# Kernel tuning notes

Measured on AMD Instinct MI355X. Metric: run time of the kernel, lower is better.

## Reference

```python
import jax, jax.numpy as jnp
import numpy as np

EMB = 1024
HEAD = 64

def setup_inputs() -> dict:
    key = jax.random.key(0)
    ks = jax.random.split(key, 7)
    s = 1.0 / np.sqrt(EMB)
    x = jax.random.normal(ks[0], (4, 2048, EMB), dtype=jnp.float32)
    Wq = jax.random.uniform(ks[1], (EMB, HEAD), jnp.float32, -s, s)
    bq = jax.random.uniform(ks[2], (HEAD,), jnp.float32, -s, s)
    Wk = jax.random.uniform(ks[3], (EMB, HEAD), jnp.float32, -s, s)
    bk = jax.random.uniform(ks[4], (HEAD,), jnp.float32, -s, s)
    Wv = jax.random.uniform(ks[5], (EMB, HEAD), jnp.float32, -s, s)
    bv = jax.random.uniform(ks[6], (HEAD,), jnp.float32, -s, s)
    return {"x": x, "Wq": Wq, "bq": bq, "Wk": Wk, "bk": bk, "Wv": Wv, "bv": bv}

def reference(x, Wq, bq, Wk, bk, Wv, bv):
    x = x.astype(jnp.float32)
    q = jnp.einsum('bse,ed->bsd', x, Wq) + bq  # [B,S,H]
    k = jnp.einsum('bse,ed->bsd', x, Wk) + bk
    v = jnp.einsum('bse,ed->bsd', x, Wv) + bv
    scale = 1.0 / jnp.sqrt(jnp.asarray(k.shape[-1], jnp.float32))
    scores = jnp.einsum('bqd,bkd->bqk', q, k) * scale  # [B,S,S]
    attn = jax.nn.softmax(scores, axis=-1)
    return jnp.einsum('bqk,bkd->bqd', attn, v)  # [B,S,H]
```

## Files before the change

kernel.cpp:

```cpp
#include <hip/hip_runtime.h>
#include <hip/hip_bf16.h>

#define ROWS_TOTAL 8192
#define EMB 1024
#define HEAD 64
#define SEQ 2048
#define KSPLIT 8
#define KC (SEQ / KSPLIT)
#define KT 64

typedef __attribute__((ext_vector_type(8))) short short8;
typedef __attribute__((ext_vector_type(4))) float f32x4;

#define MFMA16(a, b, c) __builtin_amdgcn_mfma_f32_16x16x32_bf16((a), (b), (c), 0, 0, 0)

static __device__ __forceinline__ unsigned short f2bf(float f) {
    union { float f; unsigned u; } v; v.f = f;
    unsigned r = v.u + 0x7fff + ((v.u >> 16) & 1);
    return (unsigned short)(r >> 16);
}

static __device__ __forceinline__ unsigned pk2(float a, float b) {
    __hip_bfloat162 h = __float22bfloat162_rn(float2{a, b});
    union { __hip_bfloat162 h; unsigned u; } v; v.h = h;
    return v.u;
}

__global__ __launch_bounds__(256) void wprep_kernel(
    const float* __restrict__ Wq, const float* __restrict__ Wk,
    const float* __restrict__ Wv, unsigned short* __restrict__ Wf)
{
    __shared__ float Tr[64][65];
    const int m  = blockIdx.y;
    const int k0 = blockIdx.x * 64;
    const float* __restrict__ W = (m == 0) ? Wq : (m == 1) ? Wk : Wv;
    const int t = threadIdx.x;

    #pragma unroll
    for (int j = 0; j < 4; ++j) {
        int flat = j * 1024 + t * 4;
        int k = flat >> 6, n = flat & 63;
        float4 w4 = *(const float4*)&W[(size_t)(k0 + k) * 64 + n];
        Tr[n + 0][k] = w4.x; Tr[n + 1][k] = w4.y;
        Tr[n + 2][k] = w4.z; Tr[n + 3][k] = w4.w;
    }
    __syncthreads();

    const int n   = t >> 2;
    const int k16 = t & 3;
    union { short8 s; unsigned u[4]; } o0, o1;
    #pragma unroll
    for (int i = 0; i < 4; ++i) {
        o0.u[i] = pk2(Tr[n][k16 * 16 + 2 * i],     Tr[n][k16 * 16 + 2 * i + 1]);
        o1.u[i] = pk2(Tr[n][k16 * 16 + 8 + 2 * i], Tr[n][k16 * 16 + 9 + 2 * i]);
    }
    const int tile = m * 4 + (n >> 4);
    const int ln   = n & 15;
    const int kc32 = (k0 >> 5) + (k16 >> 1);
    const int half = k16 & 1;
    size_t off = ((size_t)(kc32 * 12 + tile) * 16 + ln) * 32 + half * 16;
    *(short8*)&Wf[off]     = o0.s;
    *(short8*)&Wf[off + 8] = o1.s;
}

__global__ __launch_bounds__(512) void qkv_mfma(
    const float* __restrict__ x, const unsigned short* __restrict__ Wf,
    const float* __restrict__ bq, const float* __restrict__ bk,
    const float* __restrict__ bv,
    unsigned short* __restrict__ Qb, unsigned short* __restrict__ Kb,
    unsigned short* __restrict__ Vt)
{
    __shared__ unsigned short Xl[16][136];
    __shared__ f32x4 pr[4][3][64];
    __shared__ unsigned short vlds[64][20];

    const int t    = threadIdx.x;
    const int w    = t >> 6;
    const int lane = t & 63;
    const int ln   = lane & 15;
    const int quad = lane >> 4;
    const int m0   = blockIdx.x * 16;
    const int cg   = w >> 1;
    const int kh   = w & 1;

    const f32x4 zero = (f32x4){0.f, 0.f, 0.f, 0.f};
    f32x4 acc[3];
    #pragma unroll
    for (int j = 0; j < 3; ++j) acc[j] = zero;

    const int srow = t >> 5;
    const int scol = (t & 31) * 4;
    const float* __restrict__ xsrc = x + (size_t)(m0 + srow) * EMB + scol;

    for (int kt = 0; kt < EMB; kt += 128) {
        float4 xv = *(const float4*)(xsrc + kt);
        uint2 pk; pk.x = pk2(xv.x, xv.y); pk.y = pk2(xv.z, xv.w);
        *(uint2*)&Xl[srow][scol] = pk;
        __syncthreads();

        #pragma unroll
        for (int cc = 0; cc < 2; ++cc) {
            short8 af = *(const short8*)&Xl[ln][kh * 64 + cc * 32 + quad * 8];
            const int kc32 = (kt >> 5) + kh * 2 + cc;
            #pragma unroll
            for (int j = 0; j < 3; ++j) {
                const int tile = cg * 3 + j;
                const unsigned short* wp =
                    Wf + ((size_t)(kc32 * 12 + tile) * 16 + ln) * 32 + quad * 8;
                short8 bf = *(const short8*)wp;
                acc[j] = MFMA16(af, bf, acc[j]);
            }
        }
        __syncthreads();
    }

    if (kh == 1) {
        #pragma unroll
        for (int j = 0; j < 3; ++j) pr[cg][j][lane] = acc[j];
    }
    __syncthreads();

    if (kh == 0) {
        const float qs = 0.125f * 1.44269504f;
        #pragma unroll
        for (int j = 0; j < 3; ++j) {
            acc[j] += pr[cg][j][lane];
            const int tile = cg * 3 + j;
            const int mat  = tile >> 2;
            const int d    = (tile & 3) * 16 + ln;
            const float* bp = (mat == 0) ? bq : (mat == 1) ? bk : bv;
            const float bias = bp[d];
            #pragma unroll
            for (int r = 0; r < 4; ++r) {
                float vfull = acc[j][r] + bias;
                int row = m0 + quad * 4 + r;
                if (mat == 0)      Qb[(size_t)row * 64 + d] = f2bf(vfull * qs);
                else if (mat == 1) Kb[(size_t)row * 64 + d] = f2bf(vfull);
                else               vlds[d][quad * 4 + r] = f2bf(vfull);
            }
        }
    }
    __syncthreads();

    if (t < 256) {
        const int b  = m0 >> 11;
        const int s0 = m0 & 2047;
        const int d  = t >> 2;
        const int sq = (t & 3) * 4;
        ushort4 pk = {vlds[d][sq + 0], vlds[d][sq + 1],
                      vlds[d][sq + 2], vlds[d][sq + 3]};
        *(ushort4*)&Vt[((size_t)b * 64 + d) * SEQ + s0 + sq] = pk;
    }
}

__global__ __launch_bounds__(512) void attn_mfma(
    const unsigned short* __restrict__ Qb, const unsigned short* __restrict__ Kb,
    const unsigned short* __restrict__ Vt,
    float* __restrict__ Opart, float* __restrict__ lpart)
{
    __shared__ unsigned short Kl[KT][72];
    __shared__ unsigned short Vl[HEAD][72];
    __shared__ unsigned short Plds[8][16][72];

    const int t    = threadIdx.x;
    const int w    = t >> 6;
    const int lane = t & 63;
    const int ln   = lane & 15;
    const int quad = lane >> 4;

    const int c  = blockIdx.y;
    const int q0 = blockIdx.x * 128 + w * 16;
    const int b  = blockIdx.x >> 4;

    const unsigned short* qbase = Qb + (size_t)(q0 + ln) * 64 + quad * 8;
    short8 qa0 = *(const short8*)(qbase);
    short8 qa1 = *(const short8*)(qbase + 32);

    const f32x4 zero = (f32x4){0.f, 0.f, 0.f, 0.f};
    f32x4 O[4];
    #pragma unroll
    for (int j = 0; j < 4; ++j) O[j] = zero;
    float lacc[4] = {0.f, 0.f, 0.f, 0.f};

    const int skey = t >> 3;
    const int soff = (t & 7) * 8;
    const unsigned short* Ksrc =
        Kb + ((size_t)b * SEQ + c * KC + skey) * 64 + soff;
    const unsigned short* Vsrc =
        Vt + ((size_t)b * 64 + skey) * SEQ + c * KC + soff;

    unsigned short* P = &Plds[w][0][0];

    for (int kt = 0; kt < KC; kt += KT) {
        *(short8*)&Kl[skey][soff] = *(const short8*)(Ksrc + (size_t)kt * 64);
        *(short8*)&Vl[skey][soff] = *(const short8*)(Vsrc + kt);
        __syncthreads();

        f32x4 s[4];
        #pragma unroll
        for (int sub = 0; sub < 4; ++sub) {
            short8 kb0 = *(const short8*)&Kl[sub * 16 + ln][quad * 8];
            short8 kb1 = *(const short8*)&Kl[sub * 16 + ln][32 + quad * 8];
            s[sub] = MFMA16(qa0, kb0, zero);
            s[sub] = MFMA16(qa1, kb1, s[sub]);
        }

        #pragma unroll
        for (int r = 0; r < 4; ++r) {
            float p0 = __builtin_amdgcn_exp2f(s[0][r]);
            float p1 = __builtin_amdgcn_exp2f(s[1][r]);
            float p2 = __builtin_amdgcn_exp2f(s[2][r]);
            float p3 = __builtin_amdgcn_exp2f(s[3][r]);
            lacc[r] += (p0 + p1) + (p2 + p3);
            unsigned u01 = pk2(p0, p1);
            unsigned u23 = pk2(p2, p3);
            unsigned short* prow = P + (quad * 4 + r) * 72;
            prow[ln]      = (unsigned short)u01;
            prow[16 + ln] = (unsigned short)(u01 >> 16);
            prow[32 + ln] = (unsigned short)u23;
            prow[48 + ln] = (unsigned short)(u23 >> 16);
        }
        short8 pa0 = *(const short8*)&Plds[w][ln][quad * 8];
        short8 pa1 = *(const short8*)&Plds[w][ln][32 + quad * 8];

        #pragma unroll
        for (int j = 0; j < 4; ++j) {
            short8 vb0 = *(const short8*)&Vl[j * 16 + ln][quad * 8];
            short8 vb1 = *(const short8*)&Vl[j * 16 + ln][32 + quad * 8];
            O[j] = MFMA16(pa0, vb0, O[j]);
            O[j] = MFMA16(pa1, vb1, O[j]);
        }
        __syncthreads();
    }

    #pragma unroll
    for (int m = 1; m < 16; m <<= 1) {
        #pragma unroll
        for (int r = 0; r < 4; ++r) lacc[r] += __shfl_xor(lacc[r], m);
    }

    float* __restrict__ ob = Opart + ((size_t)c * ROWS_TOTAL + q0) * 64;
    #pragma unroll
    for (int j = 0; j < 4; ++j)
        #pragma unroll
        for (int r = 0; r < 4; ++r)
            ob[(size_t)(quad * 4 + r) * 64 + j * 16 + ln] = O[j][r];

    if (ln == 0) {
        #pragma unroll
        for (int r = 0; r < 4; ++r)
            lpart[(size_t)c * ROWS_TOTAL + q0 + quad * 4 + r] = lacc[r];
    }
}

__global__ __launch_bounds__(256) void reduce_kernel(
    const float* __restrict__ Opart, const float* __restrict__ lpart,
    float* __restrict__ out)
{
    const int idx = blockIdx.x * 256 + threadIdx.x;
    const int r   = idx >> 6;
    float osum = 0.f, lsum = 0.f;
    #pragma unroll
    for (int c = 0; c < KSPLIT; ++c) {
        osum += Opart[(size_t)c * ROWS_TOTAL * HEAD + idx];
        lsum += lpart[(size_t)c * ROWS_TOTAL + r];
    }
    out[idx] = osum / lsum;
}

extern "C" void kernel_launch(void* const* d_in, const int* in_sizes, int n_in,
                              void* d_out, int out_size, void* d_ws, size_t ws_size,
                              hipStream_t stream)
{
    const float* x  = (const float*)d_in[0];
    const float* Wq = (const float*)d_in[1];
    const float* bq = (const float*)d_in[2];
    const float* Wk = (const float*)d_in[3];
    const float* bk = (const float*)d_in[4];
    const float* Wv = (const float*)d_in[5];
    const float* bv = (const float*)d_in[6];
    float* out = (float*)d_out;

    char* ws = (char*)d_ws;
    unsigned short* Qb = (unsigned short*)ws;
    unsigned short* Kb = Qb + (size_t)ROWS_TOTAL * HEAD;
    unsigned short* Vt = Kb + (size_t)ROWS_TOTAL * HEAD;
    unsigned short* Wf = Vt + (size_t)ROWS_TOTAL * HEAD;
    float* lpart = (float*)(Wf + (size_t)3 * HEAD * EMB);
    float* Opart = lpart + (size_t)KSPLIT * ROWS_TOTAL;

    wprep_kernel<<<dim3(16, 3), 256, 0, stream>>>(Wq, Wk, Wv, Wf);
    qkv_mfma<<<dim3(512), 512, 0, stream>>>(x, Wf, bq, bk, bv, Qb, Kb, Vt);
    attn_mfma<<<dim3(64, KSPLIT), 512, 0, stream>>>(Qb, Kb, Vt, Opart, lpart);
    reduce_kernel<<<dim3((ROWS_TOTAL * HEAD) / 256), 256, 0, stream>>>(Opart, lpart, out);
}
```

Before: 118.8 us.

## Double rows per QKV block and prefetch global loads into registers

```diff
diff --git a/kernel.cpp b/kernel.cpp
--- a/kernel.cpp
+++ b/kernel.cpp
@@ -70,45 +70,57 @@
     unsigned short* __restrict__ Qb, unsigned short* __restrict__ Kb,
     unsigned short* __restrict__ Vt)
 {
-    __shared__ unsigned short Xl[16][136];
-    __shared__ f32x4 pr[4][3][64];
-    __shared__ unsigned short vlds[64][20];
+    __shared__ union {
+        unsigned short Xl[32][136];
+        f32x4 pr[4][3][2][64];
+    } sh;
+    __shared__ unsigned short vlds[64][36];
 
     const int t    = threadIdx.x;
     const int w    = t >> 6;
     const int lane = t & 63;
     const int ln   = lane & 15;
     const int quad = lane >> 4;
-    const int m0   = blockIdx.x * 16;
+    const int m0   = blockIdx.x * 32;
     const int cg   = w >> 1;
     const int kh   = w & 1;
 
     const f32x4 zero = (f32x4){0.f, 0.f, 0.f, 0.f};
-    f32x4 acc[3];
-    #pragma unroll
-    for (int j = 0; j < 3; ++j) acc[j] = zero;
-
-    const int srow = t >> 5;
-    const int scol = (t & 31) * 4;
+    f32x4 acc[3][2];
+    #pragma unroll
+    for (int j = 0; j < 3; ++j) { acc[j][0] = zero; acc[j][1] = zero; }
+
+    const int srow = t >> 4;
+    const int scol = (t & 15) * 8;
     const float* __restrict__ xsrc = x + (size_t)(m0 + srow) * EMB + scol;
 
+    float4 xa = *(const float4*)(xsrc);
+    float4 xb = *(const float4*)(xsrc + 4);
+
     for (int kt = 0; kt < EMB; kt += 128) {
-        float4 xv = *(const float4*)(xsrc + kt);
-        uint2 pk; pk.x = pk2(xv.x, xv.y); pk.y = pk2(xv.z, xv.w);
-        *(uint2*)&Xl[srow][scol] = pk;
+        union { short8 s; unsigned u[4]; } xp;
+        xp.u[0] = pk2(xa.x, xa.y); xp.u[1] = pk2(xa.z, xa.w);
+        xp.u[2] = pk2(xb.x, xb.y); xp.u[3] = pk2(xb.z, xb.w);
+        *(short8*)&sh.Xl[srow][scol] = xp.s;
         __syncthreads();
 
+        if (kt + 128 < EMB) {
+            xa = *(const float4*)(xsrc + kt + 128);
+            xb = *(const float4*)(xsrc + kt + 132);
+        }
+
         #pragma unroll
         for (int cc = 0; cc < 2; ++cc) {
-            short8 af = *(const short8*)&Xl[ln][kh * 64 + cc * 32 + quad * 8];
+            short8 af0 = *(const short8*)&sh.Xl[ln][kh * 64 + cc * 32 + quad * 8];
+            short8 af1 = *(const short8*)&sh.Xl[16 + ln][kh * 64 + cc * 32 + quad * 8];
             const int kc32 = (kt >> 5) + kh * 2 + cc;
             #pragma unroll
             for (int j = 0; j < 3; ++j) {
                 const int tile = cg * 3 + j;
-                const unsigned short* wp =
-                    Wf + ((size_t)(kc32 * 12 + tile) * 16 + ln) * 32 + quad * 8;
-                short8 bf = *(const short8*)wp;
-                acc[j] = MFMA16(af, bf, acc[j]);
+                short8 bf = *(const short8*)
+                    (Wf + ((size_t)(kc32 * 12 + tile) * 16 + ln) * 32 + quad * 8);
+                acc[j][0] = MFMA16(af0, bf, acc[j][0]);
+                acc[j][1] = MFMA16(af1, bf, acc[j][1]);
             }
         }
         __syncthreads();
@@ -116,7 +128,10 @@
 
     if (kh == 1) {
         #pragma unroll
-        for (int j = 0; j < 3; ++j) pr[cg][j][lane] = acc[j];
+        for (int j = 0; j < 3; ++j) {
+            sh.pr[cg][j][0][lane] = acc[j][0];
+            sh.pr[cg][j][1][lane] = acc[j][1];
+        }
     }
     __syncthreads();
 
@@ -124,29 +139,33 @@
         const float qs = 0.125f * 1.44269504f;
         #pragma unroll
         for (int j = 0; j < 3; ++j) {
-            acc[j] += pr[cg][j][lane];
             const int tile = cg * 3 + j;
             const int mat  = tile >> 2;
             const int d    = (tile & 3) * 16 + ln;
             const float* bp = (mat == 0) ? bq : (mat == 1) ? bk : bv;
             const float bias = bp[d];
             #pragma unroll
-            for (int r = 0; r < 4; ++r) {
-                float vfull = acc[j][r] + bias;
-                int row = m0 + quad * 4 + r;
-                if (mat == 0)      Qb[(size_t)row * 64 + d] = f2bf(vfull * qs);
-                else if (mat == 1) Kb[(size_t)row * 64 + d] = f2bf(vfull);
-                else               vlds[d][quad * 4 + r] = f2bf(vfull);
+            for (int rg = 0; rg < 2; ++rg) {
+                f32x4 s = acc[j][rg];
+                s += sh.pr[cg][j][rg][lane];
+                #pragma unroll
+                for (int r = 0; r < 4; ++r) {
+                    float vfull = s[r] + bias;
+                    int row = m0 + rg * 16 + quad * 4 + r;
+                    if (mat == 0)      Qb[(size_t)row * 64 + d] = f2bf(vfull * qs);
+                    else if (mat == 1) Kb[(size_t)row * 64 + d] = f2bf(vfull);
+                    else               vlds[d][rg * 16 + quad * 4 + r] = f2bf(vfull);
+                }
             }
         }
     }
     __syncthreads();
 
-    if (t < 256) {
+    {
         const int b  = m0 >> 11;
         const int s0 = m0 & 2047;
-        const int d  = t >> 2;
-        const int sq = (t & 3) * 4;
+        const int d  = t >> 3;
+        const int sq = (t & 7) * 4;
         ushort4 pk = {vlds[d][sq + 0], vlds[d][sq + 1],
                       vlds[d][sq + 2], vlds[d][sq + 3]};
         *(ushort4*)&Vt[((size_t)b * 64 + d) * SEQ + s0 + sq] = pk;
@@ -191,10 +210,18 @@
 
     unsigned short* P = &Plds[w][0][0];
 
+    short8 kreg = *(const short8*)(Ksrc);
+    short8 vreg = *(const short8*)(Vsrc);
+
     for (int kt = 0; kt < KC; kt += KT) {
-        *(short8*)&Kl[skey][soff] = *(const short8*)(Ksrc + (size_t)kt * 64);
-        *(short8*)&Vl[skey][soff] = *(const short8*)(Vsrc + kt);
+        *(short8*)&Kl[skey][soff] = kreg;
+        *(short8*)&Vl[skey][soff] = vreg;
         __syncthreads();
+
+        if (kt + KT < KC) {
+            kreg = *(const short8*)(Ksrc + (size_t)(kt + KT) * 64);
+            vreg = *(const short8*)(Vsrc + kt + KT);
+        }
 
         f32x4 s[4];
         #pragma unroll
@@ -290,7 +317,7 @@
     float* Opart = lpart + (size_t)KSPLIT * ROWS_TOTAL;
 
     wprep_kernel<<<dim3(16, 3), 256, 0, stream>>>(Wq, Wk, Wv, Wf);
-    qkv_mfma<<<dim3(512), 512, 0, stream>>>(x, Wf, bq, bk, bv, Qb, Kb, Vt);
+    qkv_mfma<<<dim3(256), 512, 0, stream>>>(x, Wf, bq, bk, bv, Qb, Kb, Vt);
     attn_mfma<<<dim3(64, KSPLIT), 512, 0, stream>>>(Qb, Kb, Vt, Opart, lpart);
     reduce_kernel<<<dim3((ROWS_TOTAL * HEAD) / 256), 256, 0, stream>>>(Opart, lpart, out);
 }
```

New measurement: 121.8 us. 2.5% more time.

## Store K and V in MFMA fragment layout and read them directly from global

Applied to the files above, without the earlier changes.

```diff
diff --git a/kernel.cpp b/kernel.cpp
--- a/kernel.cpp
+++ b/kernel.cpp
@@ -7,7 +7,6 @@
 #define SEQ 2048
 #define KSPLIT 8
 #define KC (SEQ / KSPLIT)
-#define KT 64
 
 typedef __attribute__((ext_vector_type(8))) short short8;
 typedef __attribute__((ext_vector_type(4))) float f32x4;
@@ -25,6 +24,7 @@
     union { __hip_bfloat162 h; unsigned u; } v; v.h = h;
     return v.u;
 }
+
 
 __global__ __launch_bounds__(256) void wprep_kernel(
     const float* __restrict__ Wq, const float* __restrict__ Wk,
@@ -67,8 +67,8 @@
     const float* __restrict__ x, const unsigned short* __restrict__ Wf,
     const float* __restrict__ bq, const float* __restrict__ bk,
     const float* __restrict__ bv,
-    unsigned short* __restrict__ Qb, unsigned short* __restrict__ Kb,
-    unsigned short* __restrict__ Vt)
+    unsigned short* __restrict__ Qb, unsigned short* __restrict__ Kf,
+    unsigned short* __restrict__ Vf)
 {
     __shared__ unsigned short Xl[16][136];
     __shared__ f32x4 pr[4][3][64];
@@ -105,9 +105,8 @@
             #pragma unroll
             for (int j = 0; j < 3; ++j) {
                 const int tile = cg * 3 + j;
-                const unsigned short* wp =
-                    Wf + ((size_t)(kc32 * 12 + tile) * 16 + ln) * 32 + quad * 8;
-                short8 bf = *(const short8*)wp;
+                short8 bf = *(const short8*)
+                    (Wf + ((size_t)(kc32 * 12 + tile) * 16 + ln) * 32 + quad * 8);
                 acc[j] = MFMA16(af, bf, acc[j]);
             }
         }
@@ -120,8 +119,12 @@
     }
     __syncthreads();
 
+    const int b2 = m0 >> 11;
+    const int s0 = m0 & 2047;
+
     if (kh == 0) {
         const float qs = 0.125f * 1.44269504f;
+        const int st = s0 >> 4;
         #pragma unroll
         for (int j = 0; j < 3; ++j) {
             acc[j] += pr[cg][j][lane];
@@ -134,33 +137,38 @@
             for (int r = 0; r < 4; ++r) {
                 float vfull = acc[j][r] + bias;
                 int row = m0 + quad * 4 + r;
-                if (mat == 0)      Qb[(size_t)row * 64 + d] = f2bf(vfull * qs);
-                else if (mat == 1) Kb[(size_t)row * 64 + d] = f2bf(vfull);
-                else               vlds[d][quad * 4 + r] = f2bf(vfull);
+                if (mat == 0) {
+                    Qb[(size_t)row * 64 + d] = f2bf(vfull * qs);
+                } else if (mat == 1) {
+                    size_t off = ((((size_t)(b2 * 128 + st) * 2 + (d >> 5)) * 16
+                                   + (quad * 4 + r)) * 4 + ((d >> 3) & 3)) * 8 + (d & 7);
+                    Kf[off] = f2bf(vfull);
+                } else {
+                    vlds[d][quad * 4 + r] = f2bf(vfull);
+                }
             }
         }
     }
     __syncthreads();
 
     if (t < 256) {
-        const int b  = m0 >> 11;
-        const int s0 = m0 & 2047;
         const int d  = t >> 2;
-        const int sq = (t & 3) * 4;
-        ushort4 pk = {vlds[d][sq + 0], vlds[d][sq + 1],
-                      vlds[d][sq + 2], vlds[d][sq + 3]};
-        *(ushort4*)&Vt[((size_t)b * 64 + d) * SEQ + s0 + sq] = pk;
+        const int kq = (t & 3) * 4;
+        const int key = s0 + kq;
+        ushort4 pk = {vlds[d][kq + 0], vlds[d][kq + 1],
+                      vlds[d][kq + 2], vlds[d][kq + 3]};
+        size_t off = ((((size_t)(b2 * 64 + (key >> 5)) * 4 + (d >> 4)) * 16
+                       + (d & 15)) * 4 + ((key >> 3) & 3)) * 8 + (key & 7);
+        *(ushort4*)&Vf[off] = pk;
     }
 }
 
 __global__ __launch_bounds__(512) void attn_mfma(
-    const unsigned short* __restrict__ Qb, const unsigned short* __restrict__ Kb,
-    const unsigned short* __restrict__ Vt,
+    const unsigned short* __restrict__ Qb, const unsigned short* __restrict__ Kf,
+    const unsigned short* __restrict__ Vf,
     float* __restrict__ Opart, float* __restrict__ lpart)
 {
-    __shared__ unsigned short Kl[KT][72];
-    __shared__ unsigned short Vl[HEAD][72];
-    __shared__ unsigned short Plds[8][16][72];
+    __shared__ unsigned short Plds[8][16][40];
 
     const int t    = threadIdx.x;
     const int w    = t >> 6;
@@ -182,55 +190,42 @@
     for (int j = 0; j < 4; ++j) O[j] = zero;
     float lacc[4] = {0.f, 0.f, 0.f, 0.f};
 
-    const int skey = t >> 3;
-    const int soff = (t & 7) * 8;
-    const unsigned short* Ksrc =
-        Kb + ((size_t)b * SEQ + c * KC + skey) * 64 + soff;
-    const unsigned short* Vsrc =
-        Vt + ((size_t)b * 64 + skey) * SEQ + c * KC + soff;
-
+    const int lnq = (ln * 4 + quad) * 8;
+    const unsigned short* Kfb = Kf + (size_t)b * 128 * 1024;
+    const unsigned short* Vfb = Vf + (size_t)b * 64 * 2048;
     unsigned short* P = &Plds[w][0][0];
 
-    for (int kt = 0; kt < KC; kt += KT) {
-        *(short8*)&Kl[skey][soff] = *(const short8*)(Ksrc + (size_t)kt * 64);
-        *(short8*)&Vl[skey][soff] = *(const short8*)(Vsrc + kt);
-        __syncthreads();
-
-        f32x4 s[4];
-        #pragma unroll
-        for (int sub = 0; sub < 4; ++sub) {
-            short8 kb0 = *(const short8*)&Kl[sub * 16 + ln][quad * 8];
-            short8 kb1 = *(const short8*)&Kl[sub * 16 + ln][32 + quad * 8];
-            s[sub] = MFMA16(qa0, kb0, zero);
-            s[sub] = MFMA16(qa1, kb1, s[sub]);
-        }
+    for (int kt = 0; kt < KC; kt += 32) {
+        const int gk    = c * KC + kt;
+        const int ktile = gk >> 4;
+        const int kch   = gk >> 5;
+
+        short8 k00 = *(const short8*)(Kfb + (size_t)ktile * 1024 + lnq);
+        short8 k01 = *(const short8*)(Kfb + (size_t)ktile * 1024 + 512 + lnq);
+        short8 k10 = *(const short8*)(Kfb + (size_t)(ktile + 1) * 1024 + lnq);
+        short8 k11 = *(const short8*)(Kfb + (size_t)(ktile + 1) * 1024 + 512 + lnq);
+
+        f32x4 sA = MFMA16(qa0, k00, zero); sA = MFMA16(qa1, k01, sA);
+        f32x4 sB = MFMA16(qa0, k10, zero); sB = MFMA16(qa1, k11, sB);
 
         #pragma unroll
         for (int r = 0; r < 4; ++r) {
-            float p0 = __builtin_amdgcn_exp2f(s[0][r]);
-            float p1 = __builtin_amdgcn_exp2f(s[1][r]);
-            float p2 = __builtin_amdgcn_exp2f(s[2][r]);
-            float p3 = __builtin_amdgcn_exp2f(s[3][r]);
-            lacc[r] += (p0 + p1) + (p2 + p3);
-            unsigned u01 = pk2(p0, p1);
-            unsigned u23 = pk2(p2, p3);
-            unsigned short* prow = P + (quad * 4 + r) * 72;
-            prow[ln]      = (unsigned short)u01;
-            prow[16 + ln] = (unsigned short)(u01 >> 16);
-            prow[32 + ln] = (unsigned short)u23;
-            prow[48 + ln] = (unsigned short)(u23 >> 16);
-        }
-        short8 pa0 = *(const short8*)&Plds[w][ln][quad * 8];
-        short8 pa1 = *(const short8*)&Plds[w][ln][32 + quad * 8];
+            float pA = __builtin_amdgcn_exp2f(sA[r]);
+            float pB = __builtin_amdgcn_exp2f(sB[r]);
+            lacc[r] += pA + pB;
+            unsigned u = pk2(pA, pB);
+            unsigned short* prow = P + (quad * 4 + r) * 40;
+            prow[ln]      = (unsigned short)u;
+            prow[16 + ln] = (unsigned short)(u >> 16);
+        }
+        short8 pa = *(const short8*)&Plds[w][ln][quad * 8];
 
         #pragma unroll
         for (int j = 0; j < 4; ++j) {
-            short8 vb0 = *(const short8*)&Vl[j * 16 + ln][quad * 8];
-            short8 vb1 = *(const short8*)&Vl[j * 16 + ln][32 + quad * 8];
-            O[j] = MFMA16(pa0, vb0, O[j]);
-            O[j] = MFMA16(pa1, vb1, O[j]);
-        }
-        __syncthreads();
+            short8 vb = *(const short8*)
+                (Vfb + (size_t)(kch * 4 + j) * 512 + lnq);
+            O[j] = MFMA16(pa, vb, O[j]);
+        }
     }
 
     #pragma unroll
@@ -283,14 +278,14 @@
 
     char* ws = (char*)d_ws;
     unsigned short* Qb = (unsigned short*)ws;
-    unsigned short* Kb = Qb + (size_t)ROWS_TOTAL * HEAD;
-    unsigned short* Vt = Kb + (size_t)ROWS_TOTAL * HEAD;
-    unsigned short* Wf = Vt + (size_t)ROWS_TOTAL * HEAD;
+    unsigned short* Kf = Qb + (size_t)ROWS_TOTAL * HEAD;
+    unsigned short* Vf = Kf + (size_t)ROWS_TOTAL * HEAD;
+    unsigned short* Wf = Vf + (size_t)ROWS_TOTAL * HEAD;
     float* lpart = (float*)(Wf + (size_t)3 * HEAD * EMB);
     float* Opart = lpart + (size_t)KSPLIT * ROWS_TOTAL;
 
     wprep_kernel<<<dim3(16, 3), 256, 0, stream>>>(Wq, Wk, Wv, Wf);
-    qkv_mfma<<<dim3(512), 512, 0, stream>>>(x, Wf, bq, bk, bv, Qb, Kb, Vt);
-    attn_mfma<<<dim3(64, KSPLIT), 512, 0, stream>>>(Qb, Kb, Vt, Opart, lpart);
+    qkv_mfma<<<dim3(512), 512, 0, stream>>>(x, Wf, bq, bk, bv, Qb, Kf, Vf);
+    attn_mfma<<<dim3(64, KSPLIT), 512, 0, stream>>>(Qb, Kf, Vf, Opart, lpart);
     reduce_kernel<<<dim3((ROWS_TOTAL * HEAD) / 256), 256, 0, stream>>>(Opart, lpart, out);
 }
```

After: 125.3 us. +5.5%, slower.

## Process two 16-row query tiles per wave in attention kernel, halving block size

Applied to the files above, without the earlier changes.

```diff
diff --git a/kernel.cpp b/kernel.cpp
--- a/kernel.cpp
+++ b/kernel.cpp
@@ -105,9 +105,8 @@
             #pragma unroll
             for (int j = 0; j < 3; ++j) {
                 const int tile = cg * 3 + j;
-                const unsigned short* wp =
-                    Wf + ((size_t)(kc32 * 12 + tile) * 16 + ln) * 32 + quad * 8;
-                short8 bf = *(const short8*)wp;
+                short8 bf = *(const short8*)
+                    (Wf + ((size_t)(kc32 * 12 + tile) * 16 + ln) * 32 + quad * 8);
                 acc[j] = MFMA16(af, bf, acc[j]);
             }
         }
@@ -153,14 +152,14 @@
     }
 }
 
-__global__ __launch_bounds__(512) void attn_mfma(
+__global__ __launch_bounds__(256) void attn_mfma(
     const unsigned short* __restrict__ Qb, const unsigned short* __restrict__ Kb,
     const unsigned short* __restrict__ Vt,
     float* __restrict__ Opart, float* __restrict__ lpart)
 {
     __shared__ unsigned short Kl[KT][72];
     __shared__ unsigned short Vl[HEAD][72];
-    __shared__ unsigned short Plds[8][16][72];
+    __shared__ unsigned short Plds[4][32][72];
 
     const int t    = threadIdx.x;
     const int w    = t >> 6;
@@ -169,66 +168,88 @@
     const int quad = lane >> 4;
 
     const int c  = blockIdx.y;
-    const int q0 = blockIdx.x * 128 + w * 16;
+    const int q0 = blockIdx.x * 128 + w * 32;
     const int b  = blockIdx.x >> 4;
 
-    const unsigned short* qbase = Qb + (size_t)(q0 + ln) * 64 + quad * 8;
-    short8 qa0 = *(const short8*)(qbase);
-    short8 qa1 = *(const short8*)(qbase + 32);
+    short8 qa0[2], qa1[2];
+    #pragma unroll
+    for (int qt = 0; qt < 2; ++qt) {
+        const unsigned short* qbase =
+            Qb + (size_t)(q0 + qt * 16 + ln) * 64 + quad * 8;
+        qa0[qt] = *(const short8*)(qbase);
+        qa1[qt] = *(const short8*)(qbase + 32);
+    }
 
     const f32x4 zero = (f32x4){0.f, 0.f, 0.f, 0.f};
-    f32x4 O[4];
-    #pragma unroll
-    for (int j = 0; j < 4; ++j) O[j] = zero;
-    float lacc[4] = {0.f, 0.f, 0.f, 0.f};
-
-    const int skey = t >> 3;
-    const int soff = (t & 7) * 8;
-    const unsigned short* Ksrc =
-        Kb + ((size_t)b * SEQ + c * KC + skey) * 64 + soff;
-    const unsigned short* Vsrc =
-        Vt + ((size_t)b * 64 + skey) * SEQ + c * KC + soff;
+    f32x4 O[2][4];
+    #pragma unroll
+    for (int qt = 0; qt < 2; ++qt)
+        #pragma unroll
+        for (int j = 0; j < 4; ++j) O[qt][j] = zero;
+    float lacc[2][4] = {};
+
+    const int r0 = t >> 3,        o0v = (t & 7) * 8;
+    const int r1 = (t + 256) >> 3, o1v = ((t + 256) & 7) * 8;
+    const unsigned short* Ksrc0 = Kb + ((size_t)b * SEQ + c * KC + r0) * 64 + o0v;
+    const unsigned short* Ksrc1 = Kb + ((size_t)b * SEQ + c * KC + r1) * 64 + o1v;
+    const unsigned short* Vsrc0 = Vt + ((size_t)b * 64 + r0) * SEQ + c * KC + o0v;
+    const unsigned short* Vsrc1 = Vt + ((size_t)b * 64 + r1) * SEQ + c * KC + o1v;
 
     unsigned short* P = &Plds[w][0][0];
 
     for (int kt = 0; kt < KC; kt += KT) {
-        *(short8*)&Kl[skey][soff] = *(const short8*)(Ksrc + (size_t)kt * 64);
-        *(short8*)&Vl[skey][soff] = *(const short8*)(Vsrc + kt);
+        *(short8*)&Kl[r0][o0v] = *(const short8*)(Ksrc0 + (size_t)kt * 64);
+        *(short8*)&Kl[r1][o1v] = *(const short8*)(Ksrc1 + (size_t)kt * 64);
+        *(short8*)&Vl[r0][o0v] = *(const short8*)(Vsrc0 + kt);
+        *(short8*)&Vl[r1][o1v] = *(const short8*)(Vsrc1 + kt);
         __syncthreads();
 
-        f32x4 s[4];
+        f32x4 s[2][4];
         #pragma unroll
         for (int sub = 0; sub < 4; ++sub) {
             short8 kb0 = *(const short8*)&Kl[sub * 16 + ln][quad * 8];
             short8 kb1 = *(const short8*)&Kl[sub * 16 + ln][32 + quad * 8];
-            s[sub] = MFMA16(qa0, kb0, zero);
-            s[sub] = MFMA16(qa1, kb1, s[sub]);
-        }
-
-        #pragma unroll
-        for (int r = 0; r < 4; ++r) {
-            float p0 = __builtin_amdgcn_exp2f(s[0][r]);
-            float p1 = __builtin_amdgcn_exp2f(s[1][r]);
-            float p2 = __builtin_amdgcn_exp2f(s[2][r]);
-            float p3 = __builtin_amdgcn_exp2f(s[3][r]);
-            lacc[r] += (p0 + p1) + (p2 + p3);
-            unsigned u01 = pk2(p0, p1);
-            unsigned u23 = pk2(p2, p3);
-            unsigned short* prow = P + (quad * 4 + r) * 72;
-            prow[ln]      = (unsigned short)u01;
-            prow[16 + ln] = (unsigned short)(u01 >> 16);
-            prow[32 + ln] = (unsigned short)u23;
-            prow[48 + ln] = (unsigned short)(u23 >> 16);
-        }
-        short8 pa0 = *(const short8*)&Plds[w][ln][quad * 8];
-        short8 pa1 = *(const short8*)&Plds[w][ln][32 + quad * 8];
+            #pragma unroll
+            for (int qt = 0; qt < 2; ++qt) {
+                s[qt][sub] = MFMA16(qa0[qt], kb0, zero);
+                s[qt][sub] = MFMA16(qa1[qt], kb1, s[qt][sub]);
+            }
+        }
+
+        #pragma unroll
+        for (int qt = 0; qt < 2; ++qt) {
+            #pragma unroll
+            for (int r = 0; r < 4; ++r) {
+                float p0 = __builtin_amdgcn_exp2f(s[qt][0][r]);
+                float p1 = __builtin_amdgcn_exp2f(s[qt][1][r]);
+                float p2 = __builtin_amdgcn_exp2f(s[qt][2][r]);
+                float p3 = __builtin_amdgcn_exp2f(s[qt][3][r]);
+                lacc[qt][r] += (p0 + p1) + (p2 + p3);
+                unsigned u01 = pk2(p0, p1);
+                unsigned u23 = pk2(p2, p3);
+                unsigned short* prow = P + (qt * 16 + quad * 4 + r) * 72;
+                prow[ln]      = (unsigned short)u01;
+                prow[16 + ln] = (unsigned short)(u01 >> 16);
+                prow[32 + ln] = (unsigned short)u23;
+                prow[48 + ln] = (unsigned short)(u23 >> 16);
+            }
+        }
+        short8 pa0[2], pa1[2];
+        #pragma unroll
+        for (int qt = 0; qt < 2; ++qt) {
+            pa0[qt] = *(const short8*)&Plds[w][qt * 16 + ln][quad * 8];
+            pa1[qt] = *(const short8*)&Plds[w][qt * 16 + ln][32 + quad * 8];
+        }
 
         #pragma unroll
         for (int j = 0; j < 4; ++j) {
             short8 vb0 = *(const short8*)&Vl[j * 16 + ln][quad * 8];
             short8 vb1 = *(const short8*)&Vl[j * 16 + ln][32 + quad * 8];
-            O[j] = MFMA16(pa0, vb0, O[j]);
-            O[j] = MFMA16(pa1, vb1, O[j]);
+            #pragma unroll
+            for (int qt = 0; qt < 2; ++qt) {
+                O[qt][j] = MFMA16(pa0[qt], vb0, O[qt][j]);
+                O[qt][j] = MFMA16(pa1[qt], vb1, O[qt][j]);
+            }
         }
         __syncthreads();
     }
@@ -236,20 +257,24 @@
     #pragma unroll
     for (int m = 1; m < 16; m <<= 1) {
         #pragma unroll
-        for (int r = 0; r < 4; ++r) lacc[r] += __shfl_xor(lacc[r], m);
-    }
-
-    float* __restrict__ ob = Opart + ((size_t)c * ROWS_TOTAL + q0) * 64;
-    #pragma unroll
-    for (int j = 0; j < 4; ++j)
-        #pragma unroll
-        for (int r = 0; r < 4; ++r)
-            ob[(size_t)(quad * 4 + r) * 64 + j * 16 + ln] = O[j][r];
-
-    if (ln == 0) {
-        #pragma unroll
-        for (int r = 0; r < 4; ++r)
-            lpart[(size_t)c * ROWS_TOTAL + q0 + quad * 4 + r] = lacc[r];
+        for (int qt = 0; qt < 2; ++qt)
+            #pragma unroll
+            for (int r = 0; r < 4; ++r) lacc[qt][r] += __shfl_xor(lacc[qt][r], m);
+    }
+
+    #pragma unroll
+    for (int qt = 0; qt < 2; ++qt) {
+        float* __restrict__ ob = Opart + ((size_t)c * ROWS_TOTAL + q0 + qt * 16) * 64;
+        #pragma unroll
+        for (int j = 0; j < 4; ++j)
+            #pragma unroll
+            for (int r = 0; r < 4; ++r)
+                ob[(size_t)(quad * 4 + r) * 64 + j * 16 + ln] = O[qt][j][r];
+        if (ln == 0) {
+            #pragma unroll
+            for (int r = 0; r < 4; ++r)
+                lpart[(size_t)c * ROWS_TOTAL + q0 + qt * 16 + quad * 4 + r] = lacc[qt][r];
+        }
     }
 }
 
@@ -291,6 +316,6 @@
 
     wprep_kernel<<<dim3(16, 3), 256, 0, stream>>>(Wq, Wk, Wv, Wf);
     qkv_mfma<<<dim3(512), 512, 0, stream>>>(x, Wf, bq, bk, bv, Qb, Kb, Vt);
-    attn_mfma<<<dim3(64, KSPLIT), 512, 0, stream>>>(Qb, Kb, Vt, Opart, lpart);
+    attn_mfma<<<dim3(64, KSPLIT), 256, 0, stream>>>(Qb, Kb, Vt, Opart, lpart);
     reduce_kernel<<<dim3((ROWS_TOTAL * HEAD) / 256), 256, 0, stream>>>(Opart, lpart, out);
 }
```

After: 118.5 us. No clear change (-0.2%).
